# Kernel optimization log

Measured on AMD Instinct MI355X. Metric: run time of the kernel, lower is better.

## Reference

```python
import jax, jax.numpy as jnp
import numpy as np

RC = 5.0  # cosine cutoff radius

def ssp(z):
    # shifted softplus, SchNet activation
    return jax.nn.softplus(z) - jnp.log(2.0).astype(z.dtype)

def setup_inputs():
    key = jax.random.key(0)
    ks = jax.random.split(key, 16)
    B, Na, Nn, G, F = 2, 2048, 48, 50, 128
    e = jax.random.normal(ks[0], (B, Na, 1), jnp.float32)
    x = jax.random.normal(ks[1], (B, Na, F), jnp.float32)
    t = jax.random.normal(ks[2], (B, Na, 1), jnp.float32)
    r_ij = jax.random.uniform(ks[3], (B, Na, Nn), jnp.float32) * 6.0  # some beyond cutoff
    neighbors = jax.random.randint(ks[4], (B, Na, Nn), 0, Na)
    pairwise_mask = jax.random.randint(ks[5], (B, Na, Nn), 0, 2).astype(jnp.int32)
    f_ij = jax.random.normal(ks[6], (B, Na, Nn, G), jnp.float32)
    def lin(k, fan_in, fan_out):
        return jax.random.normal(k, (fan_in, fan_out), jnp.float32) / np.sqrt(fan_in).astype(np.float32)
    Wf1 = lin(ks[7], G, F); bf1 = jnp.zeros((F,), jnp.float32)
    Wf2 = lin(ks[8], F, F); bf2 = jnp.zeros((F,), jnp.float32)
    Wq = lin(ks[9], F, F)
    Wk = lin(ks[10], F, F)
    Wv = lin(ks[11], F, F)
    Wo = lin(ks[12], F, F); bo = jnp.zeros((F,), jnp.float32)
    return dict(e=e, x=x, t=t, r_ij=r_ij, neighbors=neighbors, pairwise_mask=pairwise_mask,
                f_ij=f_ij, Wf1=Wf1, bf1=bf1, Wf2=Wf2, bf2=bf2, Wq=Wq, Wk=Wk, Wv=Wv, Wo=Wo, bo=bo)

def reference(e, x, t, r_ij, neighbors, pairwise_mask, f_ij,
              Wf1, bf1, Wf2, bf2, Wq, Wk, Wv, Wo, bo):
    B, Na, Nn = neighbors.shape
    F = x.shape[-1]
    # continuous filter from expanded distances: W = filter_network(2*f_ij - 1)
    W = 2.0 * f_ij - 1.0
    W = ssp(W @ Wf1 + bf1) @ Wf2 + bf2                # [B,Na,Nn,F]
    # cosine cutoff
    C = (0.5 * (jnp.cos(jnp.pi * r_ij / RC) + 1.0) * (r_ij < RC))[..., None]  # [B,Na,Nn,1]
    W = W * C
    # gather neighbor embeddings: y[b,i,n,:] = x[b, neighbors[b,i,n], :]
    idx = neighbors.reshape(B, Na * Nn)
    y = jnp.take_along_axis(x, idx[..., None], axis=1).reshape(B, Na, Nn, F)
    y_full = jnp.concatenate([x[:, :, None, :], y], axis=2)  # [B,Na,Nn+1,F] self + neighbors
    # cutoff-masked attention aggregation
    q = x @ Wq                                        # [B,Na,F]
    k = y_full @ Wk                                   # [B,Na,Nn+1,F]
    v = y_full @ Wv
    v = jnp.concatenate([v[:, :, :1, :], v[:, :, 1:, :] * W], axis=2)  # filter-modulated values
    scores = jnp.einsum('baf,banf->ban', q, k) / jnp.sqrt(jnp.float32(F))
    mask = jnp.concatenate([jnp.ones((B, Na, 1), bool), pairwise_mask.astype(bool)], axis=2)
    scores = jnp.where(mask, scores, jnp.float32(-1e9))
    attn = jax.nn.softmax(scores, axis=-1)
    m = jnp.einsum('ban,banf->baf', attn, v)
    m = ssp(m @ Wo + bo)                              # [B,Na,F]
    return (m, W)
```

## Files before the change

### kernel.cpp

```cpp
#include <hip/hip_runtime.h>

typedef unsigned int uint;
typedef unsigned short ushort;

#define B_  2
#define NA  2048
#define NN  48
#define G_  50
#define F_  128
#define NK  49
#define NROW (B_ * NA * NN)
#define NAT  (B_ * NA)

typedef short short8 __attribute__((ext_vector_type(8)));
typedef float floatx4 __attribute__((ext_vector_type(4)));

__device__ __forceinline__ float ssp(float z) {
  return fmaxf(z, 0.f) + __logf(1.f + __expf(-fabsf(z))) - 0.69314718055994531f;
}
__device__ __forceinline__ ushort f2bf(float x) {
  union { float f; uint u; } v; v.f = x;
  uint u = v.u;
  u += 0x7fffu + ((u >> 16) & 1u);
  return (ushort)(u >> 16);
}
__device__ __forceinline__ uint pk2bf(float x, float y) {
  return (uint)f2bf(x) | ((uint)f2bf(y) << 16);
}

extern "C" __global__ __launch_bounds__(256)
void prep_kernel(const float* __restrict__ Wf1, const float* __restrict__ Wf2,
                 const float* __restrict__ Wv, const float* __restrict__ Wo,
                 ushort* __restrict__ Wf1t, ushort* __restrict__ Wf2t,
                 ushort* __restrict__ Wvt, ushort* __restrict__ Wot)
{
  int gid = blockIdx.x * 256 + threadIdx.x;
  if (gid < 8192) {
    int n = gid >> 6, k = gid & 63;
    Wf1t[gid] = f2bf((k < G_) ? Wf1[(size_t)k * F_ + n] : 0.f);
  }
  for (int idx = gid; idx < 3 * 16384; idx += 24576) {
    int m = idx >> 14, e = idx & 16383;
    int n = e >> 7, k = e & 127;
    const float* src = (m == 0) ? Wf2 : (m == 1) ? Wv : Wo;
    ushort* dst = (m == 0) ? Wf2t : (m == 1) ? Wvt : Wot;
    dst[e] = f2bf(src[(size_t)k * F_ + n]);
  }
}

extern "C" __global__ __launch_bounds__(256, 4)
void qk_kernel(const float* __restrict__ x,
               const float* __restrict__ Wq, const float* __restrict__ Wk,
               float* __restrict__ Qo, float* __restrict__ Ko)
{
  __shared__ float xs[32 * 128];
  const int t = threadIdx.x;
  const int f = t & 127, h = t >> 7;
  const size_t Rb = (size_t)blockIdx.x * 32;
  const float* W = blockIdx.y ? Wk : Wq;
  float* O = blockIdx.y ? Ko : Qo;

  {
    const float4* src = (const float4*)(x + Rb * F_);
    float4* dst = (float4*)xs;
    #pragma unroll
    for (int k = 0; k < 4; ++k) dst[t + 256 * k] = src[t + 256 * k];
  }
  __syncthreads();

  float acc[16];
  #pragma unroll
  for (int j = 0; j < 16; ++j) acc[j] = 0.f;
  #pragma unroll
  for (int kc = 0; kc < 4; ++kc) {
    float wr[32];
    #pragma unroll
    for (int kk = 0; kk < 32; ++kk) wr[kk] = W[(size_t)(kc * 32 + kk) * F_ + f];
    #pragma unroll
    for (int j = 0; j < 16; ++j) {
      const float4* xr = (const float4*)&xs[(h * 16 + j) * 128 + kc * 32];
      #pragma unroll
      for (int qq = 0; qq < 8; ++qq) {
        float4 v = xr[qq];
        acc[j] += v.x * wr[qq * 4] + v.y * wr[qq * 4 + 1]
                + v.z * wr[qq * 4 + 2] + v.w * wr[qq * 4 + 3];
      }
    }
  }
  #pragma unroll
  for (int j = 0; j < 16; ++j)
    O[(Rb + h * 16 + j) * F_ + f] = acc[j];
}

extern "C" __global__ __launch_bounds__(256, 4)
void v_kernel(const float* __restrict__ x, const ushort* __restrict__ Wvt,
              float* __restrict__ Vo)
{
  __shared__ ushort xb[16 * 136];
  const int t = threadIdx.x;
  const int lane = t & 63, w = t >> 6;
  const int c16 = lane & 15, q = lane >> 4;
  const size_t Rb = (size_t)blockIdx.x * 16;

  {
    int row = t >> 4, col = (t & 15) * 8;
    float4 v0 = *(const float4*)(x + (Rb + row) * F_ + col);
    float4 v1 = *(const float4*)(x + (Rb + row) * F_ + col + 4);
    uint4 pk = { pk2bf(v0.x, v0.y), pk2bf(v0.z, v0.w),
                 pk2bf(v1.x, v1.y), pk2bf(v1.z, v1.w) };
    *(uint4*)((char*)xb + row * 272 + col * 2) = pk;
  }
  __syncthreads();

  short8 bx[4];
  const char* ap = (const char*)xb + c16 * 272 + q * 16;
  #pragma unroll
  for (int s = 0; s < 4; ++s) bx[s] = *(const short8*)(ap + s * 64);

  #pragma unroll
  for (int u = 0; u < 2; ++u) {
    int ntile = w * 2 + u;
    const char* bb = (const char*)Wvt + (ntile * 16 + c16) * 256 + q * 16;
    floatx4 acc = {0.f, 0.f, 0.f, 0.f};
    #pragma unroll
    for (int s = 0; s < 4; ++s) {
      short8 wf = *(const short8*)(bb + s * 64);
      acc = __builtin_amdgcn_mfma_f32_16x16x32_bf16(wf, bx[s], acc, 0, 0, 0);
    }
    *(floatx4*)(Vo + (Rb + c16) * F_ + ntile * 16 + q * 4) = acc;
  }
}

struct __align__(16) SmemF2 {
  union {
    ushort ft[128 * 72];
    ushort h1[128 * 136];
  } u;
  float C[128];
};

extern "C" __global__ __launch_bounds__(256, 4)
void filter_kernel(const float* __restrict__ fij, const float* __restrict__ r_ij,
                   const ushort* __restrict__ Wf1t, const float* __restrict__ bf1,
                   const ushort* __restrict__ Wf2t, const float* __restrict__ bf2p,
                   float* __restrict__ out_W)
{
  __shared__ SmemF2 sm;
  const int t = threadIdx.x;
  const int lane = t & 63, w = t >> 6;
  const int c16 = lane & 15, q = lane >> 4;
  const int m0 = w * 32;
  const size_t Rb = (size_t)blockIdx.x * 128;

  #pragma unroll
  for (int it = 0; it < 16; ++it) {
    int idx = t + it * 256;
    int row = idx >> 5, kp = idx & 31;
    uint pk = 0;
    if (kp < 25) {
      float2 v = *(const float2*)(fij + (Rb + row) * G_ + 2 * kp);
      pk = pk2bf(2.f * v.x - 1.f, 2.f * v.y - 1.f);
    }
    ((uint*)sm.u.ft)[row * 36 + kp] = pk;
  }
  if (t < 128) {
    float r = r_ij[Rb + t];
    sm.C[t] = (r < 5.0f) ? 0.5f * (cosf(0.62831853071795864769f * r) + 1.0f) : 0.0f;
  }
  __syncthreads();

  short8 a1[2][2];
  #pragma unroll
  for (int mt = 0; mt < 2; ++mt) {
    const char* ap = (const char*)sm.u.ft + (m0 + mt * 16 + c16) * 144 + q * 16;
    a1[mt][0] = *(const short8*)(ap);
    a1[mt][1] = *(const short8*)(ap + 64);
  }
  __syncthreads();

  short8 b1[8][2];
  #pragma unroll
  for (int nt = 0; nt < 8; ++nt) {
    const char* bb = (const char*)Wf1t + (nt * 16 + c16) * 128 + q * 16;
    b1[nt][0] = *(const short8*)(bb);
    b1[nt][1] = *(const short8*)(bb + 64);
  }

  #pragma unroll
  for (int nt = 0; nt < 8; ++nt) {
    int n = nt * 16 + c16;
    float bias = bf1[n];
    #pragma unroll
    for (int mt = 0; mt < 2; ++mt) {
      floatx4 acc = {0.f, 0.f, 0.f, 0.f};
      acc = __builtin_amdgcn_mfma_f32_16x16x32_bf16(a1[mt][0], b1[nt][0], acc, 0, 0, 0);
      acc = __builtin_amdgcn_mfma_f32_16x16x32_bf16(a1[mt][1], b1[nt][1], acc, 0, 0, 0);
      #pragma unroll
      for (int r = 0; r < 4; ++r) {
        int row = m0 + mt * 16 + q * 4 + r;
        sm.u.h1[row * 136 + n] = f2bf(ssp(acc[r] + bias));
      }
    }
  }

  short8 a2[2][4];
  #pragma unroll
  for (int mt = 0; mt < 2; ++mt) {
    const char* ap = (const char*)sm.u.h1 + (m0 + mt * 16 + c16) * 272 + q * 16;
    #pragma unroll
    for (int s = 0; s < 4; ++s) a2[mt][s] = *(const short8*)(ap + s * 64);
  }

  #pragma unroll
  for (int g = 0; g < 2; ++g) {
    short8 b2[4][4];
    #pragma unroll
    for (int j = 0; j < 4; ++j) {
      int n = (g * 4 + j) * 16 + c16;
      const char* bb = (const char*)Wf2t + n * 256 + q * 16;
      #pragma unroll
      for (int s = 0; s < 4; ++s) b2[j][s] = *(const short8*)(bb + s * 64);
    }
    #pragma unroll
    for (int j = 0; j < 4; ++j) {
      int n = (g * 4 + j) * 16 + c16;
      float bias = bf2p[n];
      #pragma unroll
      for (int mt = 0; mt < 2; ++mt) {
        floatx4 acc = {0.f, 0.f, 0.f, 0.f};
        #pragma unroll
        for (int s = 0; s < 4; ++s)
          acc = __builtin_amdgcn_mfma_f32_16x16x32_bf16(a2[mt][s], b2[j][s], acc, 0, 0, 0);
        #pragma unroll
        for (int r = 0; r < 4; ++r) {
          int row = m0 + mt * 16 + q * 4 + r;
          out_W[(Rb + row) * F_ + n] = (acc[r] + bias) * sm.C[row];
        }
      }
    }
  }
}

extern "C" __global__ __launch_bounds__(256, 4)
void attn_kernel(const float* __restrict__ Q, const float* __restrict__ K,
                 const float* __restrict__ V, const float* __restrict__ Wg,
                 const int* __restrict__ nbr, const int* __restrict__ pmask,
                 float* __restrict__ m_pre)
{
  const int t = threadIdx.x;
  const int lane = t & 63, w = t >> 6;
  const int a = blockIdx.x * 4 + w;
  const int b = a >> 11, i = a & 2047;
  const size_t base_nn = (size_t)a * NN;

  int nbrv = (lane < NN) ? nbr[base_nn + lane] : 0;
  int pmv  = (lane < NN) ? pmask[base_nn + lane] : 1;

  float2 q2 = *(const float2*)(Q + (size_t)a * F_ + lane * 2);

  float s_lane = -1e30f;
  #pragma unroll
  for (int n = 0; n < NK; ++n) {
    int src = (n == 0) ? i : __shfl(nbrv, (n > 0) ? n - 1 : 0);
    float2 k2 = *(const float2*)(K + ((size_t)b * NA + src) * F_ + lane * 2);
    float p = q2.x * k2.x + q2.y * k2.y;
    #pragma unroll
    for (int o = 32; o; o >>= 1) p += __shfl_xor(p, o);
    p *= 0.08838834764831845f;
    if (n > 0 && __shfl(pmv, n - 1) == 0) p = -1e9f;
    if (lane == n) s_lane = p;
  }

  float mx = s_lane;
  #pragma unroll
  for (int o = 32; o; o >>= 1) mx = fmaxf(mx, __shfl_xor(mx, o));
  float ev = (lane < NK) ? __expf(s_lane - mx) : 0.f;
  float sum = ev;
  #pragma unroll
  for (int o = 32; o; o >>= 1) sum += __shfl_xor(sum, o);
  float attn_l = ev / sum;

  float2 acc;
  {
    float a0 = __shfl(attn_l, 0);
    float2 vi = *(const float2*)(V + ((size_t)b * NA + i) * F_ + lane * 2);
    acc.x = a0 * vi.x;
    acc.y = a0 * vi.y;
  }
  for (int c = 0; c < 6; ++c) {
    float an[8];
    float2 vv[8], wv[8];
    #pragma unroll
    for (int j = 0; j < 8; ++j) {
      int n = c * 8 + j + 1;
      an[j] = __shfl(attn_l, n);
      int sr = __shfl(nbrv, n - 1);
      vv[j] = *(const float2*)(V + ((size_t)b * NA + sr) * F_ + lane * 2);
      wv[j] = *(const float2*)(Wg + (base_nn + n - 1) * F_ + lane * 2);
    }
    #pragma unroll
    for (int j = 0; j < 8; ++j) {
      acc.x += an[j] * wv[j].x * vv[j].x;
      acc.y += an[j] * wv[j].y * vv[j].y;
    }
  }
  *(float2*)(m_pre + (size_t)a * F_ + lane * 2) = acc;
}

extern "C" __global__ __launch_bounds__(256, 4)
void out_kernel(const float* __restrict__ m_pre, const ushort* __restrict__ Wot,
                const float* __restrict__ bo, float* __restrict__ out_m)
{
  __shared__ ushort xb[16 * 136];
  const int t = threadIdx.x;
  const int lane = t & 63, w = t >> 6;
  const int c16 = lane & 15, q = lane >> 4;
  const size_t Rb = (size_t)blockIdx.x * 16;

  {
    int row = t >> 4, col = (t & 15) * 8;
    float4 v0 = *(const float4*)(m_pre + (Rb + row) * F_ + col);
    float4 v1 = *(const float4*)(m_pre + (Rb + row) * F_ + col + 4);
    uint4 pk = { pk2bf(v0.x, v0.y), pk2bf(v0.z, v0.w),
                 pk2bf(v1.x, v1.y), pk2bf(v1.z, v1.w) };
    *(uint4*)((char*)xb + row * 272 + col * 2) = pk;
  }
  __syncthreads();

  short8 bx[4];
  const char* ap = (const char*)xb + c16 * 272 + q * 16;
  #pragma unroll
  for (int s = 0; s < 4; ++s) bx[s] = *(const short8*)(ap + s * 64);

  #pragma unroll
  for (int u = 0; u < 2; ++u) {
    int ntile = w * 2 + u;
    const char* bb = (const char*)Wot + (ntile * 16 + c16) * 256 + q * 16;
    floatx4 acc = {0.f, 0.f, 0.f, 0.f};
    #pragma unroll
    for (int s = 0; s < 4; ++s) {
      short8 wf = *(const short8*)(bb + s * 64);
      acc = __builtin_amdgcn_mfma_f32_16x16x32_bf16(wf, bx[s], acc, 0, 0, 0);
    }
    int n0 = ntile * 16 + q * 4;
    float4 bv = *(const float4*)&bo[n0];
    floatx4 outv;
    outv[0] = ssp(acc[0] + bv.x);
    outv[1] = ssp(acc[1] + bv.y);
    outv[2] = ssp(acc[2] + bv.z);
    outv[3] = ssp(acc[3] + bv.w);
    *(floatx4*)(out_m + (Rb + c16) * F_ + n0) = outv;
  }
}

extern "C" void kernel_launch(void* const* d_in, const int* in_sizes, int n_in,
                              void* d_out, int out_size, void* d_ws, size_t ws_size,
                              hipStream_t stream) {
  const float* x   = (const float*)d_in[1];
  const float* r   = (const float*)d_in[3];
  const int*  nbr  = (const int*)d_in[4];
  const int*  pmk  = (const int*)d_in[5];
  const float* fij = (const float*)d_in[6];
  const float* Wf1 = (const float*)d_in[7];
  const float* bf1 = (const float*)d_in[8];
  const float* Wf2 = (const float*)d_in[9];
  const float* bf2p= (const float*)d_in[10];
  const float* Wq  = (const float*)d_in[11];
  const float* Wk  = (const float*)d_in[12];
  const float* Wv  = (const float*)d_in[13];
  const float* Wo  = (const float*)d_in[14];
  const float* bo  = (const float*)d_in[15];
  float* out_m = (float*)d_out;
  float* out_W = out_m + (size_t)NAT * F_;

  float* Qs = (float*)d_ws;
  float* Ks = Qs + (size_t)NAT * F_;
  float* Vs = Ks + (size_t)NAT * F_;
  float* Ms = Vs + (size_t)NAT * F_;
  ushort* Wf1t = (ushort*)(Ms + (size_t)NAT * F_);
  ushort* Wf2t = Wf1t + 128 * 64;
  ushort* Wvt  = Wf2t + 128 * 128;
  ushort* Wot  = Wvt  + 128 * 128;

  hipLaunchKernelGGL(prep_kernel, dim3(96), dim3(256), 0, stream,
                     Wf1, Wf2, Wv, Wo, Wf1t, Wf2t, Wvt, Wot);
  hipLaunchKernelGGL(qk_kernel, dim3(NAT / 32, 2), dim3(256), 0, stream,
                     x, Wq, Wk, Qs, Ks);
  hipLaunchKernelGGL(v_kernel, dim3(NAT / 16), dim3(256), 0, stream,
                     x, Wvt, Vs);
  hipLaunchKernelGGL(filter_kernel, dim3(NROW / 128), dim3(256), 0, stream,
                     fij, r, Wf1t, bf1, Wf2t, bf2p, out_W);
  hipLaunchKernelGGL(attn_kernel, dim3(NAT / 4), dim3(256), 0, stream,
                     Qs, Ks, Vs, out_W, nbr, pmk, Ms);
  hipLaunchKernelGGL(out_kernel, dim3(NAT / 16), dim3(256), 0, stream,
                     Ms, Wot, bo, out_m);
}
```

Measured before the change: 271.1 us.

## Fuse filter network and attention aggregation into one kernel per four atoms

Merges the filter MLP and the attention kernel into one kernel. Each block handles 192 pair rows, which is exactly four atoms times 48 neighbours, using 384 threads. After the filter output is written and a barrier, four of the six waves run the attention for those atoms and read the just-written filter values while they are still cache-hot. This removes a kernel launch and the cold re-read of the large filter tensor. In exchange, two waves sit idle during the attention phase, the shared-memory footprint grows, and the gather loop is rewritten with less explicit load batching.

```diff
diff --git a/kernel.cpp b/kernel.cpp
--- a/kernel.cpp
+++ b/kernel.cpp
@@ -131,30 +131,33 @@
   }
 }
 
-struct __align__(16) SmemF2 {
+struct __align__(16) SmemFA {
   union {
-    ushort ft[128 * 72];
-    ushort h1[128 * 136];
+    ushort ft[192 * 72];
+    ushort h1[192 * 136];
   } u;
-  float C[128];
+  float C[192];
 };
 
-extern "C" __global__ __launch_bounds__(256, 4)
-void filter_kernel(const float* __restrict__ fij, const float* __restrict__ r_ij,
-                   const ushort* __restrict__ Wf1t, const float* __restrict__ bf1,
-                   const ushort* __restrict__ Wf2t, const float* __restrict__ bf2p,
-                   float* __restrict__ out_W)
-{
-  __shared__ SmemF2 sm;
+extern "C" __global__ __launch_bounds__(384, 4)
+void fused_filter_attn(const float* __restrict__ fij, const float* __restrict__ r_ij,
+                       const ushort* __restrict__ Wf1t, const float* __restrict__ bf1,
+                       const ushort* __restrict__ Wf2t, const float* __restrict__ bf2p,
+                       const float* __restrict__ Q, const float* __restrict__ K,
+                       const float* __restrict__ V,
+                       const int* __restrict__ nbr, const int* __restrict__ pmask,
+                       float* __restrict__ out_W, float* __restrict__ m_pre)
+{
+  __shared__ SmemFA sm;
   const int t = threadIdx.x;
   const int lane = t & 63, w = t >> 6;
   const int c16 = lane & 15, q = lane >> 4;
   const int m0 = w * 32;
-  const size_t Rb = (size_t)blockIdx.x * 128;
+  const size_t Rb = (size_t)blockIdx.x * 192;
 
   #pragma unroll
   for (int it = 0; it < 16; ++it) {
-    int idx = t + it * 256;
+    int idx = t + it * 384;
     int row = idx >> 5, kp = idx & 31;
     uint pk = 0;
     if (kp < 25) {
@@ -163,7 +166,7 @@
     }
     ((uint*)sm.u.ft)[row * 36 + kp] = pk;
   }
-  if (t < 128) {
+  if (t < 192) {
     float r = r_ij[Rb + t];
     sm.C[t] = (r < 5.0f) ? 0.5f * (cosf(0.62831853071795864769f * r) + 1.0f) : 0.0f;
   }
@@ -239,72 +242,54 @@
       }
     }
   }
-}
-
-extern "C" __global__ __launch_bounds__(256, 4)
-void attn_kernel(const float* __restrict__ Q, const float* __restrict__ K,
-                 const float* __restrict__ V, const float* __restrict__ Wg,
-                 const int* __restrict__ nbr, const int* __restrict__ pmask,
-                 float* __restrict__ m_pre)
-{
-  const int t = threadIdx.x;
-  const int lane = t & 63, w = t >> 6;
-  const int a = blockIdx.x * 4 + w;
-  const int b = a >> 11, i = a & 2047;
-  const size_t base_nn = (size_t)a * NN;
-
-  int nbrv = (lane < NN) ? nbr[base_nn + lane] : 0;
-  int pmv  = (lane < NN) ? pmask[base_nn + lane] : 1;
-
-  float2 q2 = *(const float2*)(Q + (size_t)a * F_ + lane * 2);
-
-  float s_lane = -1e30f;
-  #pragma unroll
-  for (int n = 0; n < NK; ++n) {
-    int src = (n == 0) ? i : __shfl(nbrv, (n > 0) ? n - 1 : 0);
-    float2 k2 = *(const float2*)(K + ((size_t)b * NA + src) * F_ + lane * 2);
-    float p = q2.x * k2.x + q2.y * k2.y;
-    #pragma unroll
-    for (int o = 32; o; o >>= 1) p += __shfl_xor(p, o);
-    p *= 0.08838834764831845f;
-    if (n > 0 && __shfl(pmv, n - 1) == 0) p = -1e9f;
-    if (lane == n) s_lane = p;
-  }
-
-  float mx = s_lane;
-  #pragma unroll
-  for (int o = 32; o; o >>= 1) mx = fmaxf(mx, __shfl_xor(mx, o));
-  float ev = (lane < NK) ? __expf(s_lane - mx) : 0.f;
-  float sum = ev;
-  #pragma unroll
-  for (int o = 32; o; o >>= 1) sum += __shfl_xor(sum, o);
-  float attn_l = ev / sum;
-
-  float2 acc;
-  {
-    float a0 = __shfl(attn_l, 0);
-    float2 vi = *(const float2*)(V + ((size_t)b * NA + i) * F_ + lane * 2);
-    acc.x = a0 * vi.x;
-    acc.y = a0 * vi.y;
-  }
-  for (int c = 0; c < 6; ++c) {
-    float an[8];
-    float2 vv[8], wv[8];
-    #pragma unroll
-    for (int j = 0; j < 8; ++j) {
-      int n = c * 8 + j + 1;
-      an[j] = __shfl(attn_l, n);
-      int sr = __shfl(nbrv, n - 1);
-      vv[j] = *(const float2*)(V + ((size_t)b * NA + sr) * F_ + lane * 2);
-      wv[j] = *(const float2*)(Wg + (base_nn + n - 1) * F_ + lane * 2);
-    }
-    #pragma unroll
-    for (int j = 0; j < 8; ++j) {
-      acc.x += an[j] * wv[j].x * vv[j].x;
-      acc.y += an[j] * wv[j].y * vv[j].y;
-    }
-  }
-  *(float2*)(m_pre + (size_t)a * F_ + lane * 2) = acc;
+
+  __syncthreads();
+  if (w < 4) {
+    const int a = blockIdx.x * 4 + w;
+    const int b = a >> 11, i = a & 2047;
+    const size_t base_nn = (size_t)a * NN;
+    const float* Wg = out_W;
+
+    int nbrv = (lane < NN) ? nbr[base_nn + lane] : 0;
+    int pmv  = (lane < NN) ? pmask[base_nn + lane] : 1;
+
+    float2 q2 = *(const float2*)(Q + (size_t)a * F_ + lane * 2);
+
+    float s_lane = -1e30f;
+    #pragma unroll
+    for (int n = 0; n < NK; ++n) {
+      int src = (n == 0) ? i : __shfl(nbrv, (n > 0) ? n - 1 : 0);
+      float2 k2 = *(const float2*)(K + ((size_t)b * NA + src) * F_ + lane * 2);
+      float p = q2.x * k2.x + q2.y * k2.y;
+      #pragma unroll
+      for (int o = 32; o; o >>= 1) p += __shfl_xor(p, o);
+      p *= 0.08838834764831845f;
+      if (n > 0 && __shfl(pmv, n - 1) == 0) p = -1e9f;
+      if (lane == n) s_lane = p;
+    }
+
+    float mx = s_lane;
+    #pragma unroll
+    for (int o = 32; o; o >>= 1) mx = fmaxf(mx, __shfl_xor(mx, o));
+    float ev = (lane < NK) ? __expf(s_lane - mx) : 0.f;
+    float sum = ev;
+    #pragma unroll
+    for (int o = 32; o; o >>= 1) sum += __shfl_xor(sum, o);
+    float attn_l = ev / sum;
+
+    float2 acc = {0.f, 0.f};
+    #pragma unroll 8
+    for (int n = 0; n < NK; ++n) {
+      float an = __shfl(attn_l, n);
+      int src = (n == 0) ? i : __shfl(nbrv, (n > 0) ? n - 1 : 0);
+      float2 v2 = *(const float2*)(V + ((size_t)b * NA + src) * F_ + lane * 2);
+      float2 w2 = {1.f, 1.f};
+      if (n > 0) w2 = *(const float2*)(Wg + (base_nn + n - 1) * F_ + lane * 2);
+      acc.x += an * w2.x * v2.x;
+      acc.y += an * w2.y * v2.y;
+    }
+    *(float2*)(m_pre + (size_t)a * F_ + lane * 2) = acc;
+  }
 }
 
 extern "C" __global__ __launch_bounds__(256, 4)
@@ -388,10 +373,9 @@
                      x, Wq, Wk, Qs, Ks);
   hipLaunchKernelGGL(v_kernel, dim3(NAT / 16), dim3(256), 0, stream,
                      x, Wvt, Vs);
-  hipLaunchKernelGGL(filter_kernel, dim3(NROW / 128), dim3(256), 0, stream,
-                     fij, r, Wf1t, bf1, Wf2t, bf2p, out_W);
-  hipLaunchKernelGGL(attn_kernel, dim3(NAT / 4), dim3(256), 0, stream,
-                     Qs, Ks, Vs, out_W, nbr, pmk, Ms);
+  hipLaunchKernelGGL(fused_filter_attn, dim3(NROW / 192), dim3(384), 0, stream,
+                     fij, r, Wf1t, bf1, Wf2t, bf2p,
+                     Qs, Ks, Vs, nbr, pmk, out_W, Ms);
   hipLaunchKernelGGL(out_kernel, dim3(NAT / 16), dim3(256), 0, stream,
                      Ms, Wot, bo, out_m);
 }
```

Result: slower. 281.9 us (+4.0%).

## Fuse attention-weighted value aggregation into filter kernel epilogue with atomics

Applied to the files above, without the earlier changes.

Splits the attention kernel into a scores/softmax pass that writes attention weights and the self term. The weighted sum of neighbor values is then folded into the filter kernel's epilogue, using the freshly computed W while it is still in registers. Per-row partials are reduced in shared memory and accumulated into m_pre with atomicAdd. This avoids re-reading the large W tensor from global memory. In exchange it adds scattered V gathers inside the filter kernel, atomic contention across blocks that share an atom, and a non-deterministic summation order.

```diff
diff --git a/kernel.cpp b/kernel.cpp
--- a/kernel.cpp
+++ b/kernel.cpp
@@ -131,19 +131,69 @@
   }
 }
 
+extern "C" __global__ __launch_bounds__(256, 4)
+void scores_kernel(const float* __restrict__ Q, const float* __restrict__ K,
+                   const float* __restrict__ V,
+                   const int* __restrict__ nbr, const int* __restrict__ pmask,
+                   float* __restrict__ attn_s, float* __restrict__ m_pre)
+{
+  const int t = threadIdx.x;
+  const int lane = t & 63, w = t >> 6;
+  const int a = blockIdx.x * 4 + w;
+  const int b = a >> 11, i = a & 2047;
+  const size_t base_nn = (size_t)a * NN;
+
+  int nbrv = (lane < NN) ? nbr[base_nn + lane] : 0;
+  int pmv  = (lane < NN) ? pmask[base_nn + lane] : 1;
+
+  float2 q2 = *(const float2*)(Q + (size_t)a * F_ + lane * 2);
+
+  float s_lane = -1e30f;
+  #pragma unroll
+  for (int n = 0; n < NK; ++n) {
+    int src = (n == 0) ? i : __shfl(nbrv, (n > 0) ? n - 1 : 0);
+    float2 k2 = *(const float2*)(K + ((size_t)b * NA + src) * F_ + lane * 2);
+    float p = q2.x * k2.x + q2.y * k2.y;
+    #pragma unroll
+    for (int o = 32; o; o >>= 1) p += __shfl_xor(p, o);
+    p *= 0.08838834764831845f;
+    if (n > 0 && __shfl(pmv, n - 1) == 0) p = -1e9f;
+    if (lane == n) s_lane = p;
+  }
+
+  float mx = s_lane;
+  #pragma unroll
+  for (int o = 32; o; o >>= 1) mx = fmaxf(mx, __shfl_xor(mx, o));
+  float ev = (lane < NK) ? __expf(s_lane - mx) : 0.f;
+  float sum = ev;
+  #pragma unroll
+  for (int o = 32; o; o >>= 1) sum += __shfl_xor(sum, o);
+  float attn_l = ev / sum;
+
+  attn_s[(size_t)a * 64 + lane] = attn_l;
+
+  float a0 = __shfl(attn_l, 0);
+  float2 vi = *(const float2*)(V + ((size_t)b * NA + i) * F_ + lane * 2);
+  float2 outv = { a0 * vi.x, a0 * vi.y };
+  *(float2*)(m_pre + (size_t)a * F_ + lane * 2) = outv;
+}
+
 struct __align__(16) SmemF2 {
   union {
     ushort ft[128 * 72];
     ushort h1[128 * 136];
+    float  pv[32 * 128];
   } u;
   float C[128];
 };
 
 extern "C" __global__ __launch_bounds__(256, 4)
-void filter_kernel(const float* __restrict__ fij, const float* __restrict__ r_ij,
-                   const ushort* __restrict__ Wf1t, const float* __restrict__ bf1,
-                   const ushort* __restrict__ Wf2t, const float* __restrict__ bf2p,
-                   float* __restrict__ out_W)
+void filter_pv_kernel(const float* __restrict__ fij, const float* __restrict__ r_ij,
+                      const ushort* __restrict__ Wf1t, const float* __restrict__ bf1,
+                      const ushort* __restrict__ Wf2t, const float* __restrict__ bf2p,
+                      const float* __restrict__ V, const float* __restrict__ attn_s,
+                      const int* __restrict__ nbr,
+                      float* __restrict__ out_W, float* __restrict__ m_pre)
 {
   __shared__ SmemF2 sm;
   const int t = threadIdx.x;
@@ -210,6 +260,20 @@
     #pragma unroll
     for (int s = 0; s < 4; ++s) a2[mt][s] = *(const short8*)(ap + s * 64);
   }
+  __syncthreads();
+
+  float attw[2][4]; int vrow[2][4];
+  #pragma unroll
+  for (int mt = 0; mt < 2; ++mt) {
+    #pragma unroll
+    for (int r = 0; r < 4; ++r) {
+      int row = m0 + mt * 16 + q * 4 + r;
+      size_t p = Rb + row;
+      int ag = (int)(p / 48), j = (int)(p % 48);
+      attw[mt][r] = attn_s[(size_t)ag * 64 + j + 1];
+      vrow[mt][r] = (ag >> 11) * NA + nbr[p];
+    }
+  }
 
   #pragma unroll
   for (int g = 0; g < 2; ++g) {
@@ -231,80 +295,35 @@
         #pragma unroll
         for (int s = 0; s < 4; ++s)
           acc = __builtin_amdgcn_mfma_f32_16x16x32_bf16(a2[mt][s], b2[j][s], acc, 0, 0, 0);
+        float s_pv = 0.f;
         #pragma unroll
         for (int r = 0; r < 4; ++r) {
           int row = m0 + mt * 16 + q * 4 + r;
-          out_W[(Rb + row) * F_ + n] = (acc[r] + bias) * sm.C[row];
+          float wv = (acc[r] + bias) * sm.C[row];
+          out_W[(Rb + row) * F_ + n] = wv;
+          float vv = V[(size_t)vrow[mt][r] * F_ + n];
+          s_pv += attw[mt][r] * wv * vv;
         }
+        int rg = (w << 3) + (mt << 2) + q;
+        sm.u.pv[rg * 128 + n] = s_pv;
       }
     }
   }
-}
-
-extern "C" __global__ __launch_bounds__(256, 4)
-void attn_kernel(const float* __restrict__ Q, const float* __restrict__ K,
-                 const float* __restrict__ V, const float* __restrict__ Wg,
-                 const int* __restrict__ nbr, const int* __restrict__ pmask,
-                 float* __restrict__ m_pre)
-{
-  const int t = threadIdx.x;
-  const int lane = t & 63, w = t >> 6;
-  const int a = blockIdx.x * 4 + w;
-  const int b = a >> 11, i = a & 2047;
-  const size_t base_nn = (size_t)a * NN;
-
-  int nbrv = (lane < NN) ? nbr[base_nn + lane] : 0;
-  int pmv  = (lane < NN) ? pmask[base_nn + lane] : 1;
-
-  float2 q2 = *(const float2*)(Q + (size_t)a * F_ + lane * 2);
-
-  float s_lane = -1e30f;
-  #pragma unroll
-  for (int n = 0; n < NK; ++n) {
-    int src = (n == 0) ? i : __shfl(nbrv, (n > 0) ? n - 1 : 0);
-    float2 k2 = *(const float2*)(K + ((size_t)b * NA + src) * F_ + lane * 2);
-    float p = q2.x * k2.x + q2.y * k2.y;
-    #pragma unroll
-    for (int o = 32; o; o >>= 1) p += __shfl_xor(p, o);
-    p *= 0.08838834764831845f;
-    if (n > 0 && __shfl(pmv, n - 1) == 0) p = -1e9f;
-    if (lane == n) s_lane = p;
-  }
-
-  float mx = s_lane;
-  #pragma unroll
-  for (int o = 32; o; o >>= 1) mx = fmaxf(mx, __shfl_xor(mx, o));
-  float ev = (lane < NK) ? __expf(s_lane - mx) : 0.f;
-  float sum = ev;
-  #pragma unroll
-  for (int o = 32; o; o >>= 1) sum += __shfl_xor(sum, o);
-  float attn_l = ev / sum;
-
-  float2 acc;
-  {
-    float a0 = __shfl(attn_l, 0);
-    float2 vi = *(const float2*)(V + ((size_t)b * NA + i) * F_ + lane * 2);
-    acc.x = a0 * vi.x;
-    acc.y = a0 * vi.y;
-  }
-  for (int c = 0; c < 6; ++c) {
-    float an[8];
-    float2 vv[8], wv[8];
-    #pragma unroll
-    for (int j = 0; j < 8; ++j) {
-      int n = c * 8 + j + 1;
-      an[j] = __shfl(attn_l, n);
-      int sr = __shfl(nbrv, n - 1);
-      vv[j] = *(const float2*)(V + ((size_t)b * NA + sr) * F_ + lane * 2);
-      wv[j] = *(const float2*)(Wg + (base_nn + n - 1) * F_ + lane * 2);
-    }
-    #pragma unroll
-    for (int j = 0; j < 8; ++j) {
-      acc.x += an[j] * wv[j].x * vv[j].x;
-      acc.y += an[j] * wv[j].y * vv[j].y;
-    }
-  }
-  *(float2*)(m_pre + (size_t)a * F_ + lane * 2) = acc;
+  __syncthreads();
+
+  const int agmin = (int)(Rb / 48);
+  const int agmax = (int)((Rb + 127) / 48);
+  const int nout = (agmax - agmin + 1) * 128;
+  for (int o = t; o < nout; o += 256) {
+    int ag = agmin + (o >> 7), f = o & 127;
+    float ssum = 0.f;
+    #pragma unroll
+    for (int rg = 0; rg < 32; ++rg) {
+      int a_of = (int)((Rb + rg * 4) / 48);
+      if (a_of == ag) ssum += sm.u.pv[rg * 128 + f];
+    }
+    atomicAdd(&m_pre[(size_t)ag * F_ + f], ssum);
+  }
 }
 
 extern "C" __global__ __launch_bounds__(256, 4)
@@ -381,6 +400,7 @@
   ushort* Wf2t = Wf1t + 128 * 64;
   ushort* Wvt  = Wf2t + 128 * 128;
   ushort* Wot  = Wvt  + 128 * 128;
+  float* As    = (float*)(Wot + 128 * 128);
 
   hipLaunchKernelGGL(prep_kernel, dim3(96), dim3(256), 0, stream,
                      Wf1, Wf2, Wv, Wo, Wf1t, Wf2t, Wvt, Wot);
@@ -388,10 +408,10 @@
                      x, Wq, Wk, Qs, Ks);
   hipLaunchKernelGGL(v_kernel, dim3(NAT / 16), dim3(256), 0, stream,
                      x, Wvt, Vs);
-  hipLaunchKernelGGL(filter_kernel, dim3(NROW / 128), dim3(256), 0, stream,
-                     fij, r, Wf1t, bf1, Wf2t, bf2p, out_W);
-  hipLaunchKernelGGL(attn_kernel, dim3(NAT / 4), dim3(256), 0, stream,
-                     Qs, Ks, Vs, out_W, nbr, pmk, Ms);
+  hipLaunchKernelGGL(scores_kernel, dim3(NAT / 4), dim3(256), 0, stream,
+                     Qs, Ks, Vs, nbr, pmk, As, Ms);
+  hipLaunchKernelGGL(filter_pv_kernel, dim3(NROW / 128), dim3(256), 0, stream,
+                     fij, r, Wf1t, bf1, Wf2t, bf2p, Vs, As, nbr, out_W, Ms);
   hipLaunchKernelGGL(out_kernel, dim3(NAT / 16), dim3(256), 0, stream,
                      Ms, Wot, bo, out_m);
 }
```

Measured after the change: 327.8 us. +20.9%, slower.
